# Optimization experiments

Measured on AMD Instinct MI355X. Metric: run time of the kernel, lower is better.

## Reference

```python
import jax, jax.numpy as jnp
import numpy as np

FIELDS, NUM, CAT = 39, 13, 26
D, M, V, B, DEEP = 16, 16, 100000, 4096, 400
LEFT, RIGHT = np.triu_indices(FIELDS, k=1)  # pair indices, Q = 741
Q = LEFT.size
EPS = 1e-5


def setup_inputs() -> dict:
    key = jax.random.key(0)
    ks = jax.random.split(key, 18)
    xi = jax.random.randint(ks[0], (B, CAT), 0, V)
    xv = jax.random.uniform(ks[1], (B, NUM), dtype=jnp.float32)
    # 2nd-order embedding tables, stacked since all fields share vocab size
    emb_tables = jax.random.normal(ks[2], (FIELDS, V, D), dtype=jnp.float32) * 0.1
    T3 = jax.random.normal(ks[3], (D, M, D), dtype=jnp.float32) * 0.05
    T2 = jax.random.normal(ks[4], (M, D * D), dtype=jnp.float32) * 0.05
    gc = jax.random.normal(ks[5], (Q,), dtype=jnp.float32)
    fi_w = jax.random.normal(ks[6], (Q * M, DEEP), dtype=jnp.float32) * 0.01
    fi_b = jnp.zeros((DEEP,), dtype=jnp.float32)
    fi_gamma = jnp.ones((DEEP,), dtype=jnp.float32)
    fi_beta = jnp.zeros((DEEP,), dtype=jnp.float32)
    emb_w = jax.random.normal(ks[7], (FIELDS * D, DEEP), dtype=jnp.float32) * 0.02
    emb_b = jnp.zeros((DEEP,), dtype=jnp.float32)
    emb_gamma = jnp.ones((DEEP,), dtype=jnp.float32)
    emb_beta = jnp.zeros((DEEP,), dtype=jnp.float32)
    fc_w = jax.random.normal(ks[8], (2 * DEEP, 1), dtype=jnp.float32) * 0.05
    fc_b = jnp.zeros((1,), dtype=jnp.float32)
    return {"xi": xi, "xv": xv, "emb_tables": emb_tables, "T3": T3, "T2": T2,
            "gc": gc, "fi_w": fi_w, "fi_b": fi_b, "fi_gamma": fi_gamma, "fi_beta": fi_beta,
            "emb_w": emb_w, "emb_b": emb_b, "emb_gamma": emb_gamma, "emb_beta": emb_beta,
            "fc_w": fc_w, "fc_b": fc_b}


def _bn(x, gamma, beta):
    # BatchNorm1d in training mode: batch statistics, biased variance
    mean = jnp.mean(x, axis=0)
    var = jnp.var(x, axis=0)
    return gamma * (x - mean) * jax.lax.rsqrt(var + EPS) + beta


def reference(xi, xv, emb_tables, T3, T2, gc, fi_w, fi_b, fi_gamma, fi_beta,
              emb_w, emb_b, emb_gamma, emb_beta, fc_w, fc_b):
    # numerical fields: embedding row 0 scaled by the raw value
    num_part = xv[:, :, None] * emb_tables[:NUM, 0, :][None]          # [B, 13, D]
    # categorical fields: per-field gather
    cat_part = emb_tables[NUM + jnp.arange(CAT)[None, :], xi]          # [B, 26, D]
    fm2 = jnp.concatenate([num_part, cat_part], axis=1)               # [B, 39, D]
    vi = fm2[:, LEFT]                                                  # [B, Q, D]
    vj = fm2[:, RIGHT]                                                 # [B, Q, D]
    # einsum('bqd,dmd,bqd->bm'): repeated d on T3 takes its diagonal -> [D, M]
    T3diag = jnp.einsum('dmd->dm', T3)
    ga = jnp.einsum('bqd,bqd,dm->bm', vi, vj, T3diag)                  # [B, M]
    ga = jax.nn.softmax(ga, axis=1)
    # T1 = einsum('bm,mn->bmn'); s = einsum('bqd,bmn,bqd->bqm') sums T1 over n
    t1_rowsum = ga * jnp.sum(T2, axis=1)[None, :]                      # [B, M]
    pair_dot = jnp.einsum('bqd,bqd->bq', vi, vj)                       # [B, Q]
    s = pair_dot[:, :, None] * t1_rowsum[:, None, :]                   # [B, Q, M]
    sh = (s * gc[None, :, None]).reshape(-1, Q * M)                    # [B, Q*M]
    th = jax.nn.relu(_bn(sh @ fi_w + fi_b, fi_gamma, fi_beta))         # [B, DEEP]
    emb = fm2.reshape(-1, FIELDS * D)                                  # [B, 39*D]
    emb = jax.nn.relu(_bn(emb @ emb_w + emb_b, emb_gamma, emb_beta))   # [B, DEEP]
    out = jnp.concatenate([th, emb], axis=1) @ fc_w + fc_b             # [B, 1]
    return jnp.sum(jax.nn.sigmoid(out), axis=1)                        # [B]
```

## Files before the change

### kernel.cpp

```cpp
#include <hip/hip_runtime.h>
#include <hip/hip_bf16.h>

#define BATCH 4096
#define FIELDS_ 39
#define NUMF 13
#define CATF 26
#define DD 16
#define MM 16
#define VV 100000
#define DEEP_ 400
#define QQ 741
#define QPAD 768
#define KE 624
#define KEP 640
#define NEP 512
#define N1 6400
#define EPS_ 1e-5f

#define OFF_ABF 0
#define OFF_T   (BATCH*QPAD/2)
#define OFF_W2  (OFF_T + BATCH*MM)
#define OFF_WE  (OFF_W2 + N1*QPAD/2)
#define OFF_FMB (OFF_WE + NEP*KEP/2)
#define OFF_TH  (OFF_FMB + BATCH*KEP/2)
#define OFF_EMB (OFF_TH + BATCH*DEEP_)
#define OFF_ACC (OFF_EMB + BATCH*DEEP_)

typedef __attribute__((ext_vector_type(8))) short bf16x8;
typedef __attribute__((ext_vector_type(4))) float f32x4;

__device__ __forceinline__ ushort f2bf(float v) {
    union { float f; unsigned u; } x; x.f = v;
    unsigned r = x.u + 0x7fff + ((x.u >> 16) & 1);
    return (ushort)(r >> 16);
}
__device__ __forceinline__ unsigned pack2(float a, float b) {
    return (unsigned)f2bf(a) | ((unsigned)f2bf(b) << 16);
}
__device__ __forceinline__ void async16(void* lds, const void* g) {
    __builtin_amdgcn_global_load_lds(
        (const __attribute__((address_space(1))) unsigned int*)g,
        (__attribute__((address_space(3))) unsigned int*)lds,
        16, 0, 0);
}

__global__ __launch_bounds__(256) void kbig(const int* __restrict__ xi,
                                            const float* __restrict__ xv,
                                            const float* __restrict__ emb,
                                            const float* __restrict__ gc,
                                            const float* __restrict__ fi_w,
                                            const float* __restrict__ emb_w,
                                            const float* __restrict__ T3,
                                            const float* __restrict__ T2,
                                            float* __restrict__ ws,
                                            ushort* __restrict__ Abf,
                                            ushort* __restrict__ FMB,
                                            ushort* __restrict__ W2,
                                            ushort* __restrict__ WE) {
    __shared__ float smem[4200];
    int bid = blockIdx.x, tid = threadIdx.x;

    if (bid < BATCH) {
        float* row = smem;
        float* hsh = smem + 624;
        float* gash = smem + 640;
        ushort* stA = (ushort*)(smem + 656);
        ushort* stF = stA + QPAD;
        int b = bid;
        for (int e = tid; e < KE; e += 256) {
            int f = e >> 4, d = e & 15;
            float v;
            if (f < NUMF) {
                v = xv[b * NUMF + f] * emb[(long)f * VV * DD + d];
            } else {
                int c = f - NUMF;
                int idxv = xi[b * CATF + c];
                v = emb[((long)(NUMF + c) * VV + idxv) * DD + d];
            }
            row[e] = v;
        }
        __syncthreads();
        for (int e = tid; e < KEP; e += 256)
            stF[e] = (e < KE) ? f2bf(row[e]) : (ushort)0;
        if (tid < DD) {
            float s = 0.f, s2 = 0.f;
            for (int f = 0; f < FIELDS_; ++f) { float v = row[f * DD + tid]; s += v; s2 += v * v; }
            hsh[tid] = 0.5f * (s * s - s2);
        }
        __syncthreads();
        if (tid < MM) {
            float g = 0.f;
            for (int d = 0; d < DD; ++d) g += hsh[d] * T3[(d * MM + tid) * DD + d];
            gash[tid] = g;
        }
        __syncthreads();
        if (tid < MM) {
            float mx = -1e30f;
            for (int m = 0; m < MM; ++m) mx = fmaxf(mx, gash[m]);
            float se = 0.f;
            for (int m = 0; m < MM; ++m) se += expf(gash[m] - mx);
            ws[OFF_T + b * MM + tid] = expf(gash[tid] - mx) / se;
        }
        for (int q = tid; q < QPAD; q += 256) {
            float av = 0.f;
            if (q < QQ) {
                int i = 0, qq = q, cnt = FIELDS_ - 1;
                while (qq >= cnt) { qq -= cnt; ++i; cnt = FIELDS_ - 1 - i; }
                int j = i + 1 + qq;
                const float4* ri = (const float4*)&row[i * DD];
                const float4* rj = (const float4*)&row[j * DD];
                float4 a0 = ri[0], a1 = ri[1], a2 = ri[2], a3 = ri[3];
                float4 b0 = rj[0], b1 = rj[1], b2 = rj[2], b3 = rj[3];
                float dot = a0.x * b0.x + a0.y * b0.y + a0.z * b0.z + a0.w * b0.w
                          + a1.x * b1.x + a1.y * b1.y + a1.z * b1.z + a1.w * b1.w
                          + a2.x * b2.x + a2.y * b2.y + a2.z * b2.z + a2.w * b2.w
                          + a3.x * b3.x + a3.y * b3.y + a3.z * b3.z + a3.w * b3.w;
                av = dot * gc[q];
            }
            stA[q] = f2bf(av);
        }
        __syncthreads();
        if (tid < 96)
            *(uint4*)&Abf[(long)b * QPAD + tid * 8] = *(uint4*)&stA[tid * 8];
        else if (tid < 176)
            *(uint4*)&FMB[(long)b * KEP + (tid - 96) * 8] = *(uint4*)&stF[(tid - 96) * 8];
    } else if (bid < BATCH + 1536) {
        int bt = bid - BATCH;
        int kt = bt >> 6, m = (bt >> 2) & 15, ch = bt & 3;
        float* tile = smem;
        {
            float p = T2[m * DD * DD + tid];
#pragma unroll
            for (int off = 32; off > 0; off >>= 1) p += __shfl_down(p, off, 64);
            if ((tid & 63) == 0) smem[4100 + (tid >> 6)] = p;
        }
        for (int i = tid; i < 32 * 25; i += 256) {
            int ql = i / 25, c4 = i - ql * 25;
            int q = kt * 32 + ql;
            float4 v = make_float4(0.f, 0.f, 0.f, 0.f);
            if (q < QQ) v = *(const float4*)&fi_w[(q * MM + m) * DEEP_ + ch * 100 + c4 * 4];
            tile[ql * 101 + c4 * 4 + 0] = v.x; tile[ql * 101 + c4 * 4 + 1] = v.y;
            tile[ql * 101 + c4 * 4 + 2] = v.z; tile[ql * 101 + c4 * 4 + 3] = v.w;
        }
        __syncthreads();
        float t2s = smem[4100] + smem[4101] + smem[4102] + smem[4103];
        for (int i = tid; i < 100 * 4; i += 256) {
            int lc = i >> 2, cq = i & 3;
            int kcol = ch * 100 + lc;
            unsigned r[4];
#pragma unroll
            for (int j = 0; j < 4; ++j)
                r[j] = pack2(tile[(cq * 8 + 2 * j) * 101 + lc] * t2s,
                             tile[(cq * 8 + 2 * j + 1) * 101 + lc] * t2s);
            *(uint4*)&W2[(long)(kcol * 16 + m) * QPAD + kt * 32 + cq * 8] =
                make_uint4(r[0], r[1], r[2], r[3]);
        }
    } else {
        int bt = bid - BATCH - 1536;
        if (bt == 0) {
            for (int i = tid; i < 1600; i += 256) ws[OFF_ACC + i] = 0.f;
        }
        int kt = bt >> 2, ch = bt & 3;
        float* tile = smem;
        for (int i = tid; i < 32 * 32; i += 256) {
            int kl = i >> 5, c4 = i & 31;
            int k = kt * 32 + kl;
            int n = ch * 128 + c4 * 4;
            float4 v = make_float4(0.f, 0.f, 0.f, 0.f);
            if (k < KE && n < DEEP_) v = *(const float4*)&emb_w[k * DEEP_ + n];
            tile[kl * 129 + c4 * 4 + 0] = v.x; tile[kl * 129 + c4 * 4 + 1] = v.y;
            tile[kl * 129 + c4 * 4 + 2] = v.z; tile[kl * 129 + c4 * 4 + 3] = v.w;
        }
        __syncthreads();
        for (int i = tid; i < 128 * 4; i += 256) {
            int nl = i >> 2, cq = i & 3;
            int n = ch * 128 + nl;
            uint4 o = make_uint4(0, 0, 0, 0);
            if (n < DEEP_) {
                unsigned r[4];
#pragma unroll
                for (int j = 0; j < 4; ++j)
                    r[j] = pack2(tile[(cq * 8 + 2 * j) * 129 + nl], tile[(cq * 8 + 2 * j + 1) * 129 + nl]);
                o = make_uint4(r[0], r[1], r[2], r[3]);
            }
            if (n < NEP)
                *(uint4*)&WE[(long)n * KEP + kt * 32 + cq * 8] = o;
        }
    }
}

__global__ __launch_bounds__(512, 1) void kgemms(const ushort* __restrict__ Abf,
                                                 const ushort* __restrict__ W2,
                                                 const ushort* __restrict__ FMB,
                                                 const ushort* __restrict__ WE,
                                                 const float* __restrict__ Tmat,
                                                 float* __restrict__ TH,
                                                 float* __restrict__ EMB,
                                                 float* __restrict__ ACC) {
    __shared__ ushort ldsbuf[65536];
    int tid = threadIdx.x;
    int lane = tid & 63, wid = tid >> 6;
    int wB = wid >> 2;
    int wS = wid & 3;
    int kq = lane >> 4, lr = lane & 15;
    f32x4 acc[8][4] = {};
    int wg = blockIdx.x;

    long stride; const ushort *m0, *m1; int ntiles;
    int b0, n0;
    bool main_ = (wg < 400);
    if (main_) {
        int L = (wg & 7) * 50 + (wg >> 3);
        n0 = (L >> 4) * 256;
        b0 = (L & 15) * 256;
        m0 = Abf + (long)b0 * QPAD;
        m1 = W2 + (long)n0 * QPAD;
        stride = QPAD; ntiles = 12;
    } else {
        int e = wg - 400;
        int se = (e & 7) * 4 + (e >> 3);
        b0 = (se >> 1) * 256;
        n0 = (se & 1) * 256;
        m0 = WE + (long)n0 * KEP;
        m1 = FMB + (long)b0 * KEP;
        stride = KEP; ntiles = 10;
    }

    int cst = tid & 7, rl = tid >> 3;
    int rowB_off = rl + ((rl & 32) ? 96 : 0);

#define STAGE1(TILE, SEG) { \
    int row_, mat_; \
    if ((SEG) < 4) { mat_ = 0; row_ = (SEG) * 64 + rl; } \
    else { mat_ = 1; row_ = ((SEG) - 4) * 32 + rowB_off; } \
    int co_ = cst ^ (row_ & 7); \
    const ushort* src_ = (mat_ ? m1 : m0) + (long)row_ * stride + (TILE) * 64 + co_ * 8; \
    async16(&ldsbuf[((TILE) & 1) * 32768 + mat_ * 16384 + row_ * 64 + cst * 8], src_); }

    int sz0 = ((kq) ^ (lr & 7)) * 8;
    int sz1 = ((4 + kq) ^ (lr & 7)) * 8;
    int a_off = (wS * 64 + lr) * 64;
    int b_off = 16384 + (wB * 128 + lr) * 64;

    bf16x8 f2r[4][2];

#define PHASE(BUFI, R, DOF2, STG, VMC) { \
    const ushort* bp_ = &ldsbuf[(BUFI) * 32768]; \
    if (DOF2) { \
        _Pragma("unroll") for (int c_ = 0; c_ < 4; ++c_) { \
            f2r[c_][0] = *(const bf16x8*)&bp_[a_off + c_ * 1024 + sz0]; \
            f2r[c_][1] = *(const bf16x8*)&bp_[a_off + c_ * 1024 + sz1]; } } \
    bf16x8 f1_[2][2]; \
    _Pragma("unroll") for (int j_ = 0; j_ < 2; ++j_) { \
        f1_[j_][0] = *(const bf16x8*)&bp_[b_off + ((R) + j_) * 1024 + sz0]; \
        f1_[j_][1] = *(const bf16x8*)&bp_[b_off + ((R) + j_) * 1024 + sz1]; } \
    STG; \
    __builtin_amdgcn_s_barrier(); \
    asm volatile("s_waitcnt lgkmcnt(0)" ::: "memory"); \
    __builtin_amdgcn_sched_barrier(0); \
    __builtin_amdgcn_s_setprio(1); \
    _Pragma("unroll") for (int j_ = 0; j_ < 2; ++j_) \
    _Pragma("unroll") for (int c_ = 0; c_ < 4; ++c_) { \
        acc[(R) + j_][c_] = __builtin_amdgcn_mfma_f32_16x16x32_bf16(f1_[j_][0], f2r[c_][0], acc[(R) + j_][c_], 0, 0, 0); \
        acc[(R) + j_][c_] = __builtin_amdgcn_mfma_f32_16x16x32_bf16(f1_[j_][1], f2r[c_][1], acc[(R) + j_][c_], 0, 0, 0); } \
    __builtin_amdgcn_s_setprio(0); \
    VMC; \
    __builtin_amdgcn_s_barrier(); }

    for (int sg = 0; sg < 8; ++sg) STAGE1(0, sg);
    for (int sg = 0; sg < 6; ++sg) STAGE1(1, sg);
    asm volatile("s_waitcnt vmcnt(6)" ::: "memory");
    __builtin_amdgcn_s_barrier();

    int niter = ntiles >> 1;
    for (int i = 0; i < niter; ++i) {
        int t0 = 2 * i, t1 = 2 * i + 1;
        bool more0 = (t0 + 2 < ntiles);
        PHASE(0, 0, true,  { STAGE1(t1, 6); STAGE1(t1, 7); }, {});
        PHASE(0, 2, false, { if (more0) { STAGE1(t0 + 2, 0); STAGE1(t0 + 2, 1); } }, {});
        PHASE(0, 4, false, { if (more0) { STAGE1(t0 + 2, 2); STAGE1(t0 + 2, 3); } }, {});
        PHASE(0, 6, false, { if (more0) { STAGE1(t0 + 2, 4); STAGE1(t0 + 2, 5); } },
              { if (more0) { asm volatile("s_waitcnt vmcnt(6)" ::: "memory"); }
                else       { asm volatile("s_waitcnt vmcnt(0)" ::: "memory"); } });
        PHASE(1, 0, true,  { if (more0) { STAGE1(t0 + 2, 6); STAGE1(t0 + 2, 7); } }, {});
        PHASE(1, 2, false, { if (more0) { STAGE1(t1 + 2, 0); STAGE1(t1 + 2, 1); } }, {});
        PHASE(1, 4, false, { if (more0) { STAGE1(t1 + 2, 2); STAGE1(t1 + 2, 3); } }, {});
        PHASE(1, 6, false, { if (more0) { STAGE1(t1 + 2, 4); STAGE1(t1 + 2, 5); } },
              { if (more0) { asm volatile("s_waitcnt vmcnt(6)" ::: "memory"); } });
    }
#undef PHASE
#undef STAGE1

    __syncthreads();
    float* red = (float*)&ldsbuf[32768];
    if (main_) {
        float* tbuf = (float*)ldsbuf;
        if (tid < 32) red[tid] = 0.f;
        __syncthreads();
        float ls[8] = {}, ls2[8] = {};
#pragma unroll
        for (int cg = 0; cg < 4; ++cg) {
            int bloc = wS * 64 + cg * 16 + lr;
            float4 t4 = *(const float4*)&Tmat[(b0 + bloc) * 16 + kq * 4];
#pragma unroll
            for (int r = 0; r < 8; ++r) {
                float v = acc[r][cg][0] * t4.x + acc[r][cg][1] * t4.y +
                          acc[r][cg][2] * t4.z + acc[r][cg][3] * t4.w;
                v += __shfl_xor(v, 16);
                v += __shfl_xor(v, 32);
                ls[r] += v; ls2[r] += v * v;
                if (lane < 16) tbuf[bloc * 17 + wB * 8 + r] = v;
            }
        }
#pragma unroll
        for (int r = 0; r < 8; ++r) {
            float a = ls[r], b2 = ls2[r];
            a += __shfl_xor(a, 8, 16); b2 += __shfl_xor(b2, 8, 16);
            a += __shfl_xor(a, 4, 16); b2 += __shfl_xor(b2, 4, 16);
            a += __shfl_xor(a, 2, 16); b2 += __shfl_xor(b2, 2, 16);
            a += __shfl_xor(a, 1, 16); b2 += __shfl_xor(b2, 1, 16);
            if (lane == 0) {
                atomicAdd(&red[wB * 8 + r], a);
                atomicAdd(&red[16 + wB * 8 + r], b2);
            }
        }
        __syncthreads();
        if (tid < 16) {
            atomicAdd(&ACC[(n0 >> 4) + tid], red[tid]);
            atomicAdd(&ACC[800 + (n0 >> 4) + tid], red[16 + tid]);
        }
        {
            int rowl = tid >> 1, kcb = (tid & 1) * 8;
            float o0 = tbuf[rowl * 17 + kcb + 0];
            float o1 = tbuf[rowl * 17 + kcb + 1];
            float o2 = tbuf[rowl * 17 + kcb + 2];
            float o3 = tbuf[rowl * 17 + kcb + 3];
            float o4 = tbuf[rowl * 17 + kcb + 4];
            float o5 = tbuf[rowl * 17 + kcb + 5];
            float o6 = tbuf[rowl * 17 + kcb + 6];
            float o7 = tbuf[rowl * 17 + kcb + 7];
            float* dst = &TH[(b0 + rowl) * DEEP_ + (n0 >> 4) + kcb];
            *(float4*)dst = make_float4(o0, o1, o2, o3);
            *(float4*)(dst + 4) = make_float4(o4, o5, o6, o7);
        }
    } else {
        red[tid] = 0.f;
        __syncthreads();
#pragma unroll
        for (int cg = 0; cg < 4; ++cg) {
            int ncl = wS * 64 + cg * 16 + lr;
            int nc = n0 + ncl;
            float ls = 0.f, ls2 = 0.f;
#pragma unroll
            for (int r = 0; r < 8; ++r) {
#pragma unroll
                for (int j = 0; j < 4; ++j) {
                    float v = acc[r][cg][j];
                    int brow = b0 + wB * 128 + r * 16 + kq * 4 + j;
                    if (nc < DEEP_) EMB[brow * DEEP_ + nc] = v;
                    ls += v; ls2 += v * v;
                }
            }
            ls += __shfl_xor(ls, 16);  ls += __shfl_xor(ls, 32);
            ls2 += __shfl_xor(ls2, 16); ls2 += __shfl_xor(ls2, 32);
            if (lane < 16 && nc < DEEP_) {
                atomicAdd(&red[ncl], ls);
                atomicAdd(&red[256 + ncl], ls2);
            }
        }
        __syncthreads();
        if (tid < 256) {
            int nc = n0 + tid;
            if (nc < DEEP_) {
                atomicAdd(&ACC[400 + nc], red[tid]);
                atomicAdd(&ACC[1200 + nc], red[256 + tid]);
            }
        }
    }
}

__global__ __launch_bounds__(256) void kfinal(const float* __restrict__ fig,
                                              const float* __restrict__ fibeta,
                                              const float* __restrict__ eg,
                                              const float* __restrict__ ebeta,
                                              const float* __restrict__ fcw,
                                              const float* __restrict__ fcb,
                                              const float* __restrict__ ws,
                                              float* __restrict__ out) {
    int b = blockIdx.x, tid = threadIdx.x;
    float part = 0.f;
    if (tid < 200) {
        int c = tid * 4;
        int loc = (c < DEEP_) ? c : c - DEEP_;
        const float* xp = (c < DEEP_) ? &ws[OFF_TH + b * DEEP_ + loc]
                                      : &ws[OFF_EMB + b * DEEP_ + loc];
        float4 x = *(const float4*)xp;
        float4 g = *(const float4*)((c < DEEP_) ? &fig[loc] : &eg[loc]);
        float4 be = *(const float4*)((c < DEEP_) ? &fibeta[loc] : &ebeta[loc]);
        float4 sm = *(const float4*)&ws[OFF_ACC + c];
        float4 sq = *(const float4*)&ws[OFF_ACC + 800 + c];
        float4 w = *(const float4*)&fcw[c];
        const float* xv_ = (const float*)&x; const float* gv = (const float*)&g;
        const float* bev = (const float*)&be; const float* smv = (const float*)&sm;
        const float* sqv = (const float*)&sq; const float* wv = (const float*)&w;
#pragma unroll
        for (int j = 0; j < 4; ++j) {
            float mean = smv[j] * (1.f / BATCH);
            float var = sqv[j] * (1.f / BATCH) - mean * mean;
            float rstd = rsqrtf(var + EPS_);
            float v = fmaxf(gv[j] * (xv_[j] - mean) * rstd + bev[j], 0.f);
            part += v * wv[j];
        }
    }
    __shared__ float red[4];
#pragma unroll
    for (int off = 32; off > 0; off >>= 1) part += __shfl_down(part, off, 64);
    if ((tid & 63) == 0) red[tid >> 6] = part;
    __syncthreads();
    if (tid == 0) {
        float tot = red[0] + red[1] + red[2] + red[3] + fcb[0];
        out[b] = 1.f / (1.f + expf(-tot));
    }
}

extern "C" void kernel_launch(void* const* d_in, const int* in_sizes, int n_in,
                              void* d_out, int out_size, void* d_ws, size_t ws_size,
                              hipStream_t stream) {
    const int*   xi    = (const int*)d_in[0];
    const float* xv    = (const float*)d_in[1];
    const float* emb   = (const float*)d_in[2];
    const float* T3    = (const float*)d_in[3];
    const float* T2    = (const float*)d_in[4];
    const float* gc    = (const float*)d_in[5];
    const float* fi_w  = (const float*)d_in[6];
    const float* fig   = (const float*)d_in[8];
    const float* fibt  = (const float*)d_in[9];
    const float* emb_w = (const float*)d_in[10];
    const float* eg    = (const float*)d_in[12];
    const float* ebt   = (const float*)d_in[13];
    const float* fcw   = (const float*)d_in[14];
    const float* fcb   = (const float*)d_in[15];
    float* ws = (float*)d_ws;
    ushort* Abf = (ushort*)(ws + OFF_ABF);
    ushort* W2  = (ushort*)(ws + OFF_W2);
    ushort* WE  = (ushort*)(ws + OFF_WE);
    ushort* FMB = (ushort*)(ws + OFF_FMB);
    float* out = (float*)d_out;

    hipLaunchKernelGGL(kbig, dim3(BATCH + 1536 + 80), dim3(256), 0, stream,
                       xi, xv, emb, gc, fi_w, emb_w, T3, T2, ws, Abf, FMB, W2, WE);
    hipLaunchKernelGGL(kgemms, dim3(432), dim3(512), 0, stream,
                       Abf, W2, FMB, WE, ws + OFF_T, ws + OFF_TH, ws + OFF_EMB, ws + OFF_ACC);
    hipLaunchKernelGGL(kfinal, dim3(BATCH), dim3(256), 0, stream,
                       fig, fibt, eg, ebt, fcw, fcb, ws, out);
}
```

Baseline: 84.41 us.

## Switch GEMM kernel from 16x16x32 to 32x32x16 bf16 MFMA tiles

Replaces the 16x16x32 MFMA instructions in the fused GEMM kernel with 32x32x16 MFMAs. LDS fragment loads, accumulator layout and both epilogues (T-contraction with BN stats, and EMB store with stats) are remapped to the 32x32 output layout. Larger MFMA tiles cut instruction count and the LDS reads per FLOP. In exchange the accumulator layout is more complex, the epilogue index math changes, and there is more risk of LDS bank conflicts with the swizzle.

```diff
diff --git a/kernel.cpp b/kernel.cpp
--- a/kernel.cpp
+++ b/kernel.cpp
@@ -27,7 +27,7 @@
 #define OFF_ACC (OFF_EMB + BATCH*DEEP_)
 
 typedef __attribute__((ext_vector_type(8))) short bf16x8;
-typedef __attribute__((ext_vector_type(4))) float f32x4;
+typedef __attribute__((ext_vector_type(16))) float f32x16;
 
 __device__ __forceinline__ ushort f2bf(float v) {
     union { float f; unsigned u; } x; x.f = v;
@@ -202,8 +202,8 @@
     int lane = tid & 63, wid = tid >> 6;
     int wB = wid >> 2;
     int wS = wid & 3;
-    int kq = lane >> 4, lr = lane & 15;
-    f32x4 acc[8][4] = {};
+    int l31 = lane & 31, h = lane >> 5, l7 = lane & 7;
+    f32x16 acc[4][2] = {};
     int wg = blockIdx.x;
 
     long stride; const ushort *m0, *m1; int ntiles;
@@ -237,32 +237,36 @@
     const ushort* src_ = (mat_ ? m1 : m0) + (long)row_ * stride + (TILE) * 64 + co_ * 8; \
     async16(&ldsbuf[((TILE) & 1) * 32768 + mat_ * 16384 + row_ * 64 + cst * 8], src_); }
 
-    int sz0 = ((kq) ^ (lr & 7)) * 8;
-    int sz1 = ((4 + kq) ^ (lr & 7)) * 8;
-    int a_off = (wS * 64 + lr) * 64;
-    int b_off = 16384 + (wB * 128 + lr) * 64;
-
-    bf16x8 f2r[4][2];
-
-#define PHASE(BUFI, R, DOF2, STG, VMC) { \
+    int pos0 = ((0 + h) ^ l7) * 8;
+    int pos1 = ((2 + h) ^ l7) * 8;
+    int pos2 = ((4 + h) ^ l7) * 8;
+    int pos3 = ((6 + h) ^ l7) * 8;
+    int a_off = (wS * 64 + l31) * 64;
+    int b_off = 16384 + (wB * 128 + l31) * 64;
+
+    bf16x8 f2r[2][4];
+
+#define PHASE(BUFI, S, DOF2, STG, VMC) { \
     const ushort* bp_ = &ldsbuf[(BUFI) * 32768]; \
     if (DOF2) { \
-        _Pragma("unroll") for (int c_ = 0; c_ < 4; ++c_) { \
-            f2r[c_][0] = *(const bf16x8*)&bp_[a_off + c_ * 1024 + sz0]; \
-            f2r[c_][1] = *(const bf16x8*)&bp_[a_off + c_ * 1024 + sz1]; } } \
-    bf16x8 f1_[2][2]; \
-    _Pragma("unroll") for (int j_ = 0; j_ < 2; ++j_) { \
-        f1_[j_][0] = *(const bf16x8*)&bp_[b_off + ((R) + j_) * 1024 + sz0]; \
-        f1_[j_][1] = *(const bf16x8*)&bp_[b_off + ((R) + j_) * 1024 + sz1]; } \
+        _Pragma("unroll") for (int t_ = 0; t_ < 2; ++t_) { \
+            f2r[t_][0] = *(const bf16x8*)&bp_[a_off + t_ * 2048 + pos0]; \
+            f2r[t_][1] = *(const bf16x8*)&bp_[a_off + t_ * 2048 + pos1]; \
+            f2r[t_][2] = *(const bf16x8*)&bp_[a_off + t_ * 2048 + pos2]; \
+            f2r[t_][3] = *(const bf16x8*)&bp_[a_off + t_ * 2048 + pos3]; } } \
+    bf16x8 f1_[4]; \
+    f1_[0] = *(const bf16x8*)&bp_[b_off + (S) * 2048 + pos0]; \
+    f1_[1] = *(const bf16x8*)&bp_[b_off + (S) * 2048 + pos1]; \
+    f1_[2] = *(const bf16x8*)&bp_[b_off + (S) * 2048 + pos2]; \
+    f1_[3] = *(const bf16x8*)&bp_[b_off + (S) * 2048 + pos3]; \
     STG; \
     __builtin_amdgcn_s_barrier(); \
     asm volatile("s_waitcnt lgkmcnt(0)" ::: "memory"); \
     __builtin_amdgcn_sched_barrier(0); \
     __builtin_amdgcn_s_setprio(1); \
-    _Pragma("unroll") for (int j_ = 0; j_ < 2; ++j_) \
-    _Pragma("unroll") for (int c_ = 0; c_ < 4; ++c_) { \
-        acc[(R) + j_][c_] = __builtin_amdgcn_mfma_f32_16x16x32_bf16(f1_[j_][0], f2r[c_][0], acc[(R) + j_][c_], 0, 0, 0); \
-        acc[(R) + j_][c_] = __builtin_amdgcn_mfma_f32_16x16x32_bf16(f1_[j_][1], f2r[c_][1], acc[(R) + j_][c_], 0, 0, 0); } \
+    _Pragma("unroll") for (int ks_ = 0; ks_ < 4; ++ks_) { \
+        acc[S][0] = __builtin_amdgcn_mfma_f32_32x32x16_bf16(f1_[ks_], f2r[0][ks_], acc[S][0], 0, 0, 0); \
+        acc[S][1] = __builtin_amdgcn_mfma_f32_32x32x16_bf16(f1_[ks_], f2r[1][ks_], acc[S][1], 0, 0, 0); } \
     __builtin_amdgcn_s_setprio(0); \
     VMC; \
     __builtin_amdgcn_s_barrier(); }
@@ -277,15 +281,15 @@
         int t0 = 2 * i, t1 = 2 * i + 1;
         bool more0 = (t0 + 2 < ntiles);
         PHASE(0, 0, true,  { STAGE1(t1, 6); STAGE1(t1, 7); }, {});
-        PHASE(0, 2, false, { if (more0) { STAGE1(t0 + 2, 0); STAGE1(t0 + 2, 1); } }, {});
-        PHASE(0, 4, false, { if (more0) { STAGE1(t0 + 2, 2); STAGE1(t0 + 2, 3); } }, {});
-        PHASE(0, 6, false, { if (more0) { STAGE1(t0 + 2, 4); STAGE1(t0 + 2, 5); } },
+        PHASE(0, 1, false, { if (more0) { STAGE1(t0 + 2, 0); STAGE1(t0 + 2, 1); } }, {});
+        PHASE(0, 2, false, { if (more0) { STAGE1(t0 + 2, 2); STAGE1(t0 + 2, 3); } }, {});
+        PHASE(0, 3, false, { if (more0) { STAGE1(t0 + 2, 4); STAGE1(t0 + 2, 5); } },
               { if (more0) { asm volatile("s_waitcnt vmcnt(6)" ::: "memory"); }
                 else       { asm volatile("s_waitcnt vmcnt(0)" ::: "memory"); } });
         PHASE(1, 0, true,  { if (more0) { STAGE1(t0 + 2, 6); STAGE1(t0 + 2, 7); } }, {});
-        PHASE(1, 2, false, { if (more0) { STAGE1(t1 + 2, 0); STAGE1(t1 + 2, 1); } }, {});
-        PHASE(1, 4, false, { if (more0) { STAGE1(t1 + 2, 2); STAGE1(t1 + 2, 3); } }, {});
-        PHASE(1, 6, false, { if (more0) { STAGE1(t1 + 2, 4); STAGE1(t1 + 2, 5); } },
+        PHASE(1, 1, false, { if (more0) { STAGE1(t1 + 2, 0); STAGE1(t1 + 2, 1); } }, {});
+        PHASE(1, 2, false, { if (more0) { STAGE1(t1 + 2, 2); STAGE1(t1 + 2, 3); } }, {});
+        PHASE(1, 3, false, { if (more0) { STAGE1(t1 + 2, 4); STAGE1(t1 + 2, 5); } },
               { if (more0) { asm volatile("s_waitcnt vmcnt(6)" ::: "memory"); } });
     }
 #undef PHASE
@@ -299,29 +303,38 @@
         __syncthreads();
         float ls[8] = {}, ls2[8] = {};
 #pragma unroll
-        for (int cg = 0; cg < 4; ++cg) {
-            int bloc = wS * 64 + cg * 16 + lr;
-            float4 t4 = *(const float4*)&Tmat[(b0 + bloc) * 16 + kq * 4];
-#pragma unroll
-            for (int r = 0; r < 8; ++r) {
-                float v = acc[r][cg][0] * t4.x + acc[r][cg][1] * t4.y +
-                          acc[r][cg][2] * t4.z + acc[r][cg][3] * t4.w;
-                v += __shfl_xor(v, 16);
-                v += __shfl_xor(v, 32);
-                ls[r] += v; ls2[r] += v * v;
-                if (lane < 16) tbuf[bloc * 17 + wB * 8 + r] = v;
-            }
-        }
-#pragma unroll
-        for (int r = 0; r < 8; ++r) {
-            float a = ls[r], b2 = ls2[r];
-            a += __shfl_xor(a, 8, 16); b2 += __shfl_xor(b2, 8, 16);
-            a += __shfl_xor(a, 4, 16); b2 += __shfl_xor(b2, 4, 16);
-            a += __shfl_xor(a, 2, 16); b2 += __shfl_xor(b2, 2, 16);
-            a += __shfl_xor(a, 1, 16); b2 += __shfl_xor(b2, 1, 16);
+        for (int t = 0; t < 2; ++t) {
+            int bloc = wS * 64 + t * 32 + l31;
+            float4 t4a = *(const float4*)&Tmat[(b0 + bloc) * 16 + 4 * h];
+            float4 t4b = *(const float4*)&Tmat[(b0 + bloc) * 16 + 8 + 4 * h];
+            const float* ta = (const float*)&t4a;
+            const float* tb = (const float*)&t4b;
+#pragma unroll
+            for (int s = 0; s < 4; ++s) {
+#pragma unroll
+                for (int c = 0; c < 2; ++c) {
+                    int br = c * 8;
+                    float v = acc[s][t][br + 0] * ta[0] + acc[s][t][br + 1] * ta[1]
+                            + acc[s][t][br + 2] * ta[2] + acc[s][t][br + 3] * ta[3]
+                            + acc[s][t][br + 4] * tb[0] + acc[s][t][br + 5] * tb[1]
+                            + acc[s][t][br + 6] * tb[2] + acc[s][t][br + 7] * tb[3];
+                    v += __shfl_xor(v, 32);
+                    ls[s * 2 + c] += v; ls2[s * 2 + c] += v * v;
+                    if (lane < 32) tbuf[bloc * 17 + wB * 8 + s * 2 + c] = v;
+                }
+            }
+        }
+#pragma unroll
+        for (int idx = 0; idx < 8; ++idx) {
+            float a = ls[idx], b2 = ls2[idx];
+            a += __shfl_xor(a, 1, 32);  b2 += __shfl_xor(b2, 1, 32);
+            a += __shfl_xor(a, 2, 32);  b2 += __shfl_xor(b2, 2, 32);
+            a += __shfl_xor(a, 4, 32);  b2 += __shfl_xor(b2, 4, 32);
+            a += __shfl_xor(a, 8, 32);  b2 += __shfl_xor(b2, 8, 32);
+            a += __shfl_xor(a, 16, 32); b2 += __shfl_xor(b2, 16, 32);
             if (lane == 0) {
-                atomicAdd(&red[wB * 8 + r], a);
-                atomicAdd(&red[16 + wB * 8 + r], b2);
+                atomicAdd(&red[wB * 8 + idx], a);
+                atomicAdd(&red[16 + wB * 8 + idx], b2);
             }
         }
         __syncthreads();
@@ -347,23 +360,22 @@
         red[tid] = 0.f;
         __syncthreads();
 #pragma unroll
-        for (int cg = 0; cg < 4; ++cg) {
-            int ncl = wS * 64 + cg * 16 + lr;
+        for (int t = 0; t < 2; ++t) {
+            int ncl = wS * 64 + t * 32 + l31;
             int nc = n0 + ncl;
             float ls = 0.f, ls2 = 0.f;
 #pragma unroll
-            for (int r = 0; r < 8; ++r) {
-#pragma unroll
-                for (int j = 0; j < 4; ++j) {
-                    float v = acc[r][cg][j];
-                    int brow = b0 + wB * 128 + r * 16 + kq * 4 + j;
+            for (int s = 0; s < 4; ++s) {
+#pragma unroll
+                for (int reg = 0; reg < 16; ++reg) {
+                    float v = acc[s][t][reg];
+                    int row32 = (reg & 3) + 8 * (reg >> 2) + 4 * h;
+                    int brow = b0 + wB * 128 + s * 32 + row32;
                     if (nc < DEEP_) EMB[brow * DEEP_ + nc] = v;
                     ls += v; ls2 += v * v;
                 }
             }
-            ls += __shfl_xor(ls, 16);  ls += __shfl_xor(ls, 32);
-            ls2 += __shfl_xor(ls2, 16); ls2 += __shfl_xor(ls2, 32);
-            if (lane < 16 && nc < DEEP_) {
+            if (nc < DEEP_) {
                 atomicAdd(&red[ncl], ls);
                 atomicAdd(&red[256 + ncl], ls2);
             }
```

After: 87.28 us. 3.4% more time.
